# Kernel tuning notes

Hardware: AMD Instinct MI355X
Metric: run time of the kernel (lower is better)

## Reference

```python
import jax, jax.numpy as jnp
import numpy as np

E = 512
H = 8
SL = (16, 16, 16)
B = 4
LEN = np.array([768, 640, 704, 600], dtype=np.int32)


def _starts(lengths):
    cs = jnp.cumsum(lengths)
    starts = jnp.concatenate([jnp.zeros((1,), cs.dtype), cs[:-1]])
    return starts, cs


def _tile_within(data, lengths, buffer):
    # per-token causal window [cur, cur-1, ..., cur-L]; slots before sample start come from buffer
    L = buffer.shape[0]
    N = data.shape[0]
    starts, cs = _starts(lengths)
    g = jnp.arange(N)
    sid = jnp.searchsorted(cs, g, side='right')
    qpos = g - starts[sid]
    src = qpos[:, None] - jnp.arange(L + 1)[None, :]  # [N, L+1]
    from_data = src >= 0
    didx = jnp.clip(starts[sid][:, None] + src, 0, N - 1)
    bidx = jnp.clip(L + src, 0, L - 1)
    return jnp.where(from_data[:, :, None], data[didx], buffer[bidx])


def _mlp(h, w1, b1, w2, b2):
    return jax.nn.gelu(h @ w1 + b1, approximate=False) @ w2 + b2


def _selection(eu, lengths, win):
    # faithful port of the no_grad selection block (B > 1 branch)
    N = eu.shape[0]
    starts, _ = _starts(lengths)
    ends = starts + lengths - 1
    running = jnp.cumsum(eu)
    end_u = running[ends]
    sample_u = jnp.concatenate([end_u[:1], end_u[2:] - end_u[1:-1]])
    running = running - jnp.cumsum(jnp.zeros((N,), eu.dtype).at[starts[1:]].set(sample_u))
    offs = jnp.cumsum(jnp.zeros((N,), eu.dtype).at[starts[1:]].set(lengths[:-1].astype(eu.dtype)))
    idxs = jnp.arange(1, N + 1, dtype=eu.dtype) - offs
    selected = (eu > running / idxs) | (idxs <= win)
    csel = jnp.cumsum(selected.astype(jnp.int32))
    end_counts = csel[ends]
    next_lengths = jnp.concatenate([end_counts[:1], end_counts[1:] - end_counts[:-1]])
    take_map = csel - csel[0]  # unique_consecutive inverse of a 0/1-increment cumsum
    return jnp.nonzero(selected)[0], next_lengths, take_map


def _forward(args, lengths, sels):
    (x, kv_w, kv_b, q_w, q_b, proj_w, proj_b, buf0, buf1, buf2,
     d0_w1, d0_b1, d0_w2, d0_b2, d1_w1, d1_b1, d1_w2, d1_b2,
     u0_w1, u0_b1, u0_w2, u0_b2, u1_w1, u1_b1, u1_w2, u1_b2,
     wq, bq, wk, bk, wv, bv, out_w, out_b) = args
    Ls = [int(v) for v in np.asarray(lengths)]
    x_flat = jnp.concatenate([x[b, :Ls[b]] for b in range(len(Ls))])  # [N0, E]
    kv0 = x_flat @ kv_w + kv_b  # [N0, 2E]
    # scale 0
    tiled0 = _tile_within(kv0, lengths, buf0)  # [N0, SL0, 2E]
    eu0 = jax.nn.elu(_mlp(tiled0.reshape(tiled0.shape[0], -1), u0_w1, u0_b1, u0_w2, u0_b2))[:, 0] + 1.0
    s0 = _selection(jax.lax.stop_gradient(eu0), lengths, SL[0]) if sels is None else sels[0]
    sel0, len1, tm0 = s0
    selt0 = jnp.take(tiled0, sel0, 0)
    r0 = jax.nn.softmax(_mlp(selt0.reshape(selt0.shape[0], -1), d0_w1, d0_b1, d0_w2, d0_b2), -1)
    dat1 = jnp.sum(selt0 * r0[:, :, None], -2)  # [N1, 2E]
    util0 = _tile_within(jnp.take(eu0, sel0, 0)[:, None], len1, jnp.zeros((SL[1] - 1, 1), eu0.dtype))
    # scale 1
    tiled1 = _tile_within(dat1, len1, buf1)  # [N1, SL1, 2E]
    eu1 = jax.nn.elu(_mlp(tiled1.reshape(tiled1.shape[0], -1), u1_w1, u1_b1, u1_w2, u1_b2))[:, 0] + 1.0
    s1 = _selection(jax.lax.stop_gradient(eu1), len1, SL[1]) if sels is None else sels[1]
    sel1, len2, tm1 = s1
    selt1 = jnp.take(tiled1, sel1, 0)
    r1 = jax.nn.softmax(_mlp(selt1.reshape(selt1.shape[0], -1), d1_w1, d1_b1, d1_w2, d1_b2), -1)
    dat2 = jnp.sum(selt1 * r1[:, :, None], -2)  # [N2, 2E]
    util1 = _tile_within(jnp.take(eu1, sel1, 0)[:, None], len2, jnp.zeros((SL[2] - 1, 1), eu1.dtype))
    tiled2 = _tile_within(dat2, len2, buf2)  # [N2, SL2, 2E]
    # per-token multi-scale kv context (reconstructed tail of truncated forward)
    idx1 = tm0
    idx2 = jnp.take(tm1, idx1)
    win1 = jnp.take(tiled1, idx1, 0) * jnp.take(util0, idx1, 0)
    win2 = jnp.take(tiled2, idx2, 0) * jnp.take(util1, idx2, 0)
    kv = jnp.concatenate([tiled0, win1, win2], 1)  # [N0, sum(SL), 2E]
    k = kv[..., :E]
    v = kv[..., E:]
    q = x_flat @ q_w + q_b
    N0 = q.shape[0]
    Skv = kv.shape[1]
    hd = E // H
    qh = (q @ wq + bq).reshape(N0, H, hd)
    kh = (k @ wk + bk).reshape(N0, Skv, H, hd)
    vh = (v @ wv + bv).reshape(N0, Skv, H, hd)
    attn = jax.nn.softmax(jnp.einsum('nhd,nshd->nhs', qh, kh) / float(np.sqrt(hd)), -1)
    ctx = jnp.einsum('nhs,nshd->nhd', attn, vh).reshape(N0, E)
    y = (ctx @ out_w + out_b) @ proj_w + proj_b  # dropout in eval mode == identity
    out = jnp.zeros((len(Ls), max(Ls), E), y.dtype)
    off = 0
    for b, Lb in enumerate(Ls):
        out = out.at[b, :Lb].set(y[off:off + Lb])
        off += Lb
    return out, (s0, s1)


def setup_inputs():
    ks = list(jax.random.split(jax.random.key(0), 64))
    it = iter(ks)

    def nrm(shape, s=0.02):
        return jax.random.normal(next(it), shape, jnp.float32) * s

    def uni(shape):
        return jax.random.uniform(next(it), shape, dtype=jnp.float32)

    F = 2 * E
    inp = {
        'x': jax.random.normal(next(it), (B, int(LEN.max()), E), jnp.float32),
        'lengths': jnp.array(LEN),
        'kv_w': nrm((E, F)), 'kv_b': jnp.zeros((F,), jnp.float32),
        'q_w': nrm((E, E)), 'q_b': jnp.zeros((E,), jnp.float32),
        'proj_w': nrm((E, E)), 'proj_b': jnp.zeros((E,), jnp.float32),
        'buf0': uni((SL[0] - 1, F)), 'buf1': uni((SL[1] - 1, F)), 'buf2': uni((SL[2] - 1, F)),
    }
    for li in (0, 1):
        sl = SL[li]
        din, hid = sl * F, sl * 10
        inp['d%d_w1' % li] = nrm((din, hid)); inp['d%d_b1' % li] = jnp.zeros((hid,), jnp.float32)
        inp['d%d_w2' % li] = nrm((hid, sl)); inp['d%d_b2' % li] = jnp.zeros((sl,), jnp.float32)
        inp['u%d_w1' % li] = nrm((din, hid)); inp['u%d_b1' % li] = jnp.zeros((hid,), jnp.float32)
        inp['u%d_w2' % li] = nrm((hid, 1)); inp['u%d_b2' % li] = jnp.zeros((1,), jnp.float32)
    inp.update({'wq': nrm((E, E)), 'bq': jnp.zeros((E,), jnp.float32),
                'wk': nrm((E, E)), 'bk': jnp.zeros((E,), jnp.float32),
                'wv': nrm((E, E)), 'bv': jnp.zeros((E,), jnp.float32),
                'out_w': nrm((E, E)), 'out_b': jnp.zeros((E,), jnp.float32)})
    return inp


def reference(x, lengths, kv_w, kv_b, q_w, q_b, proj_w, proj_b, buf0, buf1, buf2,
              d0_w1, d0_b1, d0_w2, d0_b2, d1_w1, d1_b1, d1_w2, d1_b2,
              u0_w1, u0_b1, u0_w2, u0_b2, u1_w1, u1_b1, u1_w2, u1_b2,
              wq, bq, wk, bk, wv, bv, out_w, out_b):
    args = (x, kv_w, kv_b, q_w, q_b, proj_w, proj_b, buf0, buf1, buf2,
            d0_w1, d0_b1, d0_w2, d0_b2, d1_w1, d1_b1, d1_w2, d1_b2,
            u0_w1, u0_b1, u0_w2, u0_b2, u1_w1, u1_b1, u1_w2, u1_b2,
            wq, bq, wk, bk, wv, bv, out_w, out_b)
    out, _ = _forward(args, lengths, None)
    return out
```

## Files before the change

### kernel.cpp

```cpp
#include <hip/hip_runtime.h>
#include <cstddef>

#define DEVFN __device__ __forceinline__

constexpr int N0   = 2712;
constexpr int MAXL = 768;
constexpr int NBAT = 4;
constexpr int E    = 512;
constexpr int F    = 1024;
constexpr int HID  = 160;
constexpr int WSZ  = 16;
constexpr int NY   = 2 * WSZ * HID;
constexpr int XSTR = 2560;
constexpr size_t NOFF = (size_t)-1;

constexpr size_t oXF    = 0;
constexpr size_t oXO    = oXF    + (size_t)N0*E;
constexpr size_t oEU0   = oXO    + (size_t)N0*XSTR;
constexpr size_t oDAT1  = oEU0   + (size_t)N0;
constexpr size_t oEU1   = oDAT1  + (size_t)N0*F;
constexpr size_t oDAT2  = oEU1   + (size_t)N0;
constexpr size_t oBH0K  = oDAT2  + (size_t)N0*F;
constexpr size_t oBH0V  = oBH0K  + (size_t)15*E;
constexpr size_t oDH1K  = oBH0V  + (size_t)15*E;
constexpr size_t oDH1V  = oDH1K  + (size_t)N0*E;
constexpr size_t oDH2K  = oDH1V  + (size_t)N0*E;
constexpr size_t oDH2V  = oDH2K  + (size_t)N0*E;
constexpr size_t oCTX   = oDH2V  + (size_t)N0*E;
constexpr size_t oY2    = oCTX   + (size_t)N0*E;
constexpr size_t oEUS0  = oY2    + (size_t)N0*E;
constexpr size_t oEUS1  = oEUS0  + (size_t)N0;
constexpr size_t oSEL0  = oEUS1  + (size_t)N0;
constexpr size_t oTM0   = oSEL0  + (size_t)N0;
constexpr size_t oSEL1  = oTM0   + (size_t)N0;
constexpr size_t oTM1   = oSEL1  + (size_t)N0;
constexpr size_t oB0    = oTM1   + (size_t)N0;
constexpr size_t oB1    = oB0    + 8;
constexpr size_t oB2    = oB1    + 8;
constexpr size_t oWOP   = oB2    + 8;
constexpr size_t oBOP   = oWOP   + (size_t)E*E;
constexpr size_t oWX    = oBOP   + E;
constexpr size_t oXB    = oWX    + (size_t)E*XSTR;
constexpr size_t oBD0   = oXB    + XSTR;
constexpr size_t oBD1   = oBD0   + (size_t)F*NY;
constexpr size_t oBUFY0 = oBD1   + (size_t)F*NY;
constexpr size_t oBUFY1 = oBUFY0 + (size_t)15*NY;
constexpr size_t oYB    = oBUFY1 + (size_t)15*NY;
constexpr size_t oEND   = oYB    + (size_t)N0*NY;

__device__ float g_pool[oEND];

DEVFN float geluf(float x) {
    return 0.5f * x * (1.0f + erff(x / 1.41421356237309504880f));
}

__global__ void k_init() {
    if (threadIdx.x == 0) {
        int* b = (int*)(g_pool + oB0);
        b[0] = 0; b[1] = 768; b[2] = 1408; b[3] = 2112; b[4] = N0;
    }
}

__global__ __launch_bounds__(256) void k_xflat(const float* __restrict__ x) {
    int idx = blockIdx.x * 256 + threadIdx.x;
    if (idx >= N0 * E) return;
    int d = idx & (E - 1);
    int g = idx >> 9;
    int s = (g >= 768) + (g >= 1408) + (g >= 2112);
    const int st[4] = {0, 768, 1408, 2112};
    int qp = g - st[s];
    g_pool[oXF + idx] = x[((size_t)s * MAXL + qp) * E + d];
}

__global__ __launch_bounds__(256) void k_reshape(
    const float* __restrict__ uw, const float* __restrict__ dw, size_t bdOff)
{
    int idx = blockIdx.x * 256 + threadIdx.x;
    if (idx >= F * NY) return;
    int col = idx % NY;
    int f = idx / NY;
    const float* src = (col < NY / 2) ? uw : dw;
    int rem = (col < NY / 2) ? col : col - NY / 2;
    int j = rem / HID, n = rem % HID;
    g_pool[bdOff + idx] = src[((size_t)j * F + f) * HID + n];
}

__global__ __launch_bounds__(256) void k_copymat(
    const float* __restrict__ src, size_t dstOff, int rows, int cols, int lds, int ldd)
{
    int idx = blockIdx.x * 256 + threadIdx.x;
    if (idx >= rows * cols) return;
    int r = idx / cols, c = idx % cols;
    g_pool[dstOff + (size_t)r * ldd + c] = src[(size_t)r * lds + c];
}

__global__ __launch_bounds__(256) void k_prepvec(
    const float* __restrict__ kv_b, const float* __restrict__ q_b, const float* __restrict__ out_b,
    const float* __restrict__ wk, const float* __restrict__ bk,
    const float* __restrict__ wv, const float* __restrict__ bv,
    const float* __restrict__ wq, const float* __restrict__ bq,
    const float* __restrict__ proj_w, const float* __restrict__ proj_b)
{
    int idx = blockIdx.x * 256 + threadIdx.x;
    if (idx >= 3072) return;
    if (idx < 1024) { g_pool[oXB + idx] = kv_b[idx]; return; }
    const float* vec; const float* W; const float* add; int n; size_t dst;
    if (idx < 1536)      { n = idx - 1024; vec = kv_b;     W = wk;     add = bk;     dst = oXB + idx; }
    else if (idx < 2048) { n = idx - 1536; vec = kv_b + E; W = wv;     add = bv;     dst = oXB + idx; }
    else if (idx < 2560) { n = idx - 2048; vec = q_b;      W = wq;     add = bq;     dst = oXB + idx; }
    else                 { n = idx - 2560; vec = out_b;    W = proj_w; add = proj_b; dst = oBOP + n; }
    float s = add[n];
    for (int k = 0; k < E; ++k) s = fmaf(vec[k], W[(size_t)k * E + n], s);
    g_pool[dst] = s;
}

DEVFN void gemm64_body(
    const float* __restrict__ A, int lda,
    const float* __restrict__ B, int ldb,
    const float* __restrict__ bias,
    float* __restrict__ C, int ldc,
    int mval, int row0, int col0, int K, int N)
{
    __shared__ __align__(16) float As[32][68];
    __shared__ __align__(16) float Bs[32][64];

    int tid = threadIdx.x;
    float acc[4][4] = {};
    int tx = tid & 15, ty = tid >> 4;

    for (int k0 = 0; k0 < K; k0 += 32) {
        #pragma unroll
        for (int l = 0; l < 8; ++l) {
            int idx = tid + l * 256;
            int kk = idx & 31, m = idx >> 5;
            int r = row0 + m;
            float v = 0.0f;
            if (r < mval) v = A[(size_t)r * lda + k0 + kk];
            As[kk][m] = v;
        }
        #pragma unroll
        for (int l = 0; l < 8; ++l) {
            int idx = tid + l * 256;
            int n = idx & 63, kk = idx >> 6;
            int col = col0 + n;
            float v = 0.0f;
            if (col < N) v = B[(size_t)(k0 + kk) * ldb + col];
            Bs[kk][n] = v;
        }
        __syncthreads();
        #pragma unroll
        for (int kk = 0; kk < 32; ++kk) {
            float4 a4 = *(const float4*)&As[kk][ty * 4];
            float4 b4 = *(const float4*)&Bs[kk][tx * 4];
            float av[4] = {a4.x, a4.y, a4.z, a4.w};
            float bv[4] = {b4.x, b4.y, b4.z, b4.w};
            #pragma unroll
            for (int i = 0; i < 4; ++i)
                #pragma unroll
                for (int jn = 0; jn < 4; ++jn)
                    acc[i][jn] = fmaf(av[i], bv[jn], acc[i][jn]);
        }
        __syncthreads();
    }

    #pragma unroll
    for (int i = 0; i < 4; ++i) {
        int r = row0 + ty * 4 + i;
        if (r >= mval) continue;
        #pragma unroll
        for (int jn = 0; jn < 4; ++jn) {
            int col = col0 + tx * 4 + jn;
            if (col < N)
                C[(size_t)r * ldc + col] = acc[i][jn] + (bias ? bias[col] : 0.0f);
        }
    }
}

__global__ __launch_bounds__(256) void k_pgemm(
    size_t Aoff, int lda, size_t Boff, int ldb, size_t biasOff,
    size_t Coff, int ldc, int M, size_t mdevOff, int K, int N)
{
    int mval = (mdevOff == NOFF) ? M : *(const int*)(g_pool + mdevOff);
    int row0 = blockIdx.x * 64, col0 = blockIdx.y * 64;
    if (row0 >= mval) return;
    gemm64_body(g_pool + Aoff, lda, g_pool + Boff, ldb,
                (biasOff == NOFF) ? nullptr : g_pool + biasOff,
                g_pool + Coff, ldc, mval, row0, col0, K, N);
}

__global__ __launch_bounds__(256) void k_wprep(
    const float* __restrict__ kv_w, const float* __restrict__ q_w, const float* __restrict__ out_w,
    const float* __restrict__ wk, const float* __restrict__ wv,
    const float* __restrict__ wq, const float* __restrict__ proj_w)
{
    int z = blockIdx.z;
    const float* A; int lda; const float* B; float* C; int ldc;
    if (z == 0)      { A = kv_w;     lda = F; B = wk;     C = g_pool + oWX + 1024; ldc = XSTR; }
    else if (z == 1) { A = kv_w + E; lda = F; B = wv;     C = g_pool + oWX + 1536; ldc = XSTR; }
    else if (z == 2) { A = q_w;      lda = E; B = wq;     C = g_pool + oWX + 2048; ldc = XSTR; }
    else             { A = out_w;    lda = E; B = proj_w; C = g_pool + oWOP;       ldc = E;    }
    gemm64_body(A, lda, B, E, nullptr, C, ldc, E, blockIdx.x * 64, blockIdx.y * 64, E, E);
}

__global__ __launch_bounds__(256) void k_bufy(
    const float* __restrict__ buf0, const float* __restrict__ buf1)
{
    int z = blockIdx.z;
    const float* A = z ? buf1 : buf0;
    const float* B = g_pool + (z ? oBD1 : oBD0);
    float* C = g_pool + (z ? oBUFY1 : oBUFY0);
    gemm64_body(A, F, B, NY, nullptr, C, NY, 15, 0, blockIdx.y * 64, F, NY);
}

__global__ __launch_bounds__(256) void k_bh(
    const float* __restrict__ buf0,
    const float* __restrict__ wk, const float* __restrict__ bk,
    const float* __restrict__ wv, const float* __restrict__ bv)
{
    int z = blockIdx.z;
    const float* A = buf0 + (size_t)z * E;
    const float* B = z ? wv : wk;
    const float* bias = z ? bv : bk;
    float* C = g_pool + (z ? oBH0V : oBH0K);
    gemm64_body(A, F, B, E, bias, C, E, 15, 0, blockIdx.y * 64, E, E);
}

DEVFN void gemm128_body(
    const float* __restrict__ A, int lda,
    const float* __restrict__ B, int ldb,
    const float* __restrict__ bias,
    float* __restrict__ C, int ldc,
    int mval, int row0, int col0, int K)
{
    __shared__ __align__(16) float As[16][132];
    __shared__ __align__(16) float Bs[16][128];

    int tid = threadIdx.x;
    int tx = tid & 15, ty = tid >> 4;
    float acc[16][8] = {};

    for (int k0 = 0; k0 < K; k0 += 16) {
        #pragma unroll
        for (int l = 0; l < 4; ++l) {
            int idx = tid + l * 128;
            int r = idx >> 2, kq = (idx & 3) * 4;
            float4 v = make_float4(0.f, 0.f, 0.f, 0.f);
            int rr = row0 + r;
            if (rr < mval) v = *(const float4*)&A[(size_t)rr * lda + k0 + kq];
            As[kq][r] = v.x; As[kq + 1][r] = v.y; As[kq + 2][r] = v.z; As[kq + 3][r] = v.w;
        }
        #pragma unroll
        for (int l = 0; l < 4; ++l) {
            int idx = tid + l * 128;
            int k = idx >> 5, nq = (idx & 31) * 4;
            *(float4*)&Bs[k][nq] = *(const float4*)&B[(size_t)(k0 + k) * ldb + col0 + nq];
        }
        __syncthreads();
        #pragma unroll
        for (int kk = 0; kk < 16; ++kk) {
            float a0[16], b0[8];
            *(float4*)&a0[0]  = *(const float4*)&As[kk][ty * 16];
            *(float4*)&a0[4]  = *(const float4*)&As[kk][ty * 16 + 4];
            *(float4*)&a0[8]  = *(const float4*)&As[kk][ty * 16 + 8];
            *(float4*)&a0[12] = *(const float4*)&As[kk][ty * 16 + 12];
            *(float4*)&b0[0] = *(const float4*)&Bs[kk][tx * 4];
            *(float4*)&b0[4] = *(const float4*)&Bs[kk][64 + tx * 4];
            #pragma unroll
            for (int i = 0; i < 16; ++i)
                #pragma unroll
                for (int jn = 0; jn < 8; ++jn)
                    acc[i][jn] = fmaf(a0[i], b0[jn], acc[i][jn]);
        }
        __syncthreads();
    }

    #pragma unroll
    for (int i = 0; i < 16; ++i) {
        int r = row0 + ty * 16 + i;
        if (r >= mval) continue;
        float o0[4], o1[4];
        #pragma unroll
        for (int jn = 0; jn < 4; ++jn) {
            o0[jn] = acc[i][jn]     + (bias ? bias[col0 + tx * 4 + jn]      : 0.0f);
            o1[jn] = acc[i][jn + 4] + (bias ? bias[col0 + 64 + tx * 4 + jn] : 0.0f);
        }
        *(float4*)&C[(size_t)r * ldc + col0 + tx * 4]      = *(float4*)&o0[0];
        *(float4*)&C[(size_t)r * ldc + col0 + 64 + tx * 4] = *(float4*)&o1[0];
    }
}

__global__ __launch_bounds__(128, 2) void k_tgemm(
    size_t Aoff, int lda, size_t Boff, int ldb, size_t biasOff,
    size_t Coff, int ldc, int M, size_t mdevOff, int K)
{
    int mval = (mdevOff == NOFF) ? M : *(const int*)(g_pool + mdevOff);
    int row0 = blockIdx.x * 128, col0 = blockIdx.y * 128;
    if (row0 >= mval) return;
    gemm128_body(g_pool + Aoff, lda, g_pool + Boff, ldb,
                 (biasOff == NOFF) ? nullptr : g_pool + biasOff,
                 g_pool + Coff, ldc, mval, row0, col0, K);
}

__global__ __launch_bounds__(256) void k_zgemm(
    const float* __restrict__ wk, const float* __restrict__ wv)
{
    int z = blockIdx.z;
    int mval = *(const int*)(g_pool + ((z < 2) ? (oB1 + 4) : (oB2 + 4)));
    int row0 = blockIdx.x * 64, col0 = blockIdx.y * 64;
    if (row0 >= mval) return;
    const float* A = g_pool + ((z < 2) ? oDAT1 : oDAT2) + (size_t)(z & 1) * E;
    const float* B = (z & 1) ? wv : wk;
    float* C = g_pool + oDH1K + (size_t)z * N0 * E;
    gemm64_body(A, F, B, E, nullptr, C, E, mval, row0, col0, E, E);
}

__global__ void k_huev(
    size_t boundsOff, size_t bufYOff,
    const float* __restrict__ b1, const float* __restrict__ w2, const float* __restrict__ b2,
    size_t euOff, size_t mdevOff, int M)
{
    int i = blockIdx.x;
    int mval = (mdevOff == NOFF) ? M : *(const int*)(g_pool + mdevOff);
    if (i >= mval) return;
    int n = threadIdx.x;

    __shared__ float t[HID];
    const int* bounds = (const int*)(g_pool + boundsOff);
    int b1i = bounds[1], b2i = bounds[2], b3i = bounds[3];
    int s = (i >= b1i) + (i >= b2i) + (i >= b3i);
    int st = (s == 0) ? 0 : ((s == 1) ? b1i : ((s == 2) ? b2i : b3i));
    int qp = i - st;

    const float* Y = g_pool + oYB;
    const float* bufY = g_pool + bufYOff;

    if (n < HID) {
        float acc = b1[n];
        #pragma unroll
        for (int j = 0; j < WSZ; ++j) {
            int sp = qp - j;
            const float* row = (sp >= 0) ? &Y[(size_t)(i - j) * NY]
                                         : &bufY[(size_t)(15 + sp) * NY];
            acc += row[j * HID + n];
        }
        t[n] = geluf(acc) * w2[n];
    }
    __syncthreads();
    if (n == 0) {
        float v = b2[0];
        for (int k = 0; k < HID; ++k) v += t[k];
        v = (v > 0.0f) ? v : expm1f(v);
        g_pool[euOff + i] = v + 1.0f;
    }
}

__global__ __launch_bounds__(256) void k_select(
    size_t euOff, size_t boundsOff, int win,
    size_t selOff, size_t tmOff, size_t euSelOff, size_t boundsNextOff)
{
    __shared__ __align__(16) float se[N0];
    __shared__ __align__(16) float run[N0];
    __shared__ int sFlag[N0];
    __shared__ int sSum[256];
    __shared__ float sCz[NBAT];
    __shared__ int sEc[NBAT];
    __shared__ int sB[5];

    int tid = threadIdx.x;
    const int* bounds = (const int*)(g_pool + boundsOff);
    if (tid < 5) sB[tid] = bounds[tid];
    __syncthreads();
    int N = sB[4];
    for (int i = tid; i < N; i += 256) se[i] = g_pool[euOff + i];
    __syncthreads();

    if (tid == 0) {
        float r = 0.0f;
        int g = 0;
        for (; g + 8 <= N; g += 8) {
            float4 a = *(const float4*)&se[g];
            float4 b4 = *(const float4*)&se[g + 4];
            r += a.x;  run[g]     = r;
            r += a.y;  run[g + 1] = r;
            r += a.z;  run[g + 2] = r;
            r += a.w;  run[g + 3] = r;
            r += b4.x; run[g + 4] = r;
            r += b4.y; run[g + 5] = r;
            r += b4.z; run[g + 6] = r;
            r += b4.w; run[g + 7] = r;
        }
        for (; g < N; ++g) { r += se[g]; run[g] = r; }
        float e0 = run[sB[1] - 1], e1 = run[sB[2] - 1], e2 = run[sB[3] - 1];
        float su0 = e0;
        float su1 = e2 - e1;
        float su2 = run[sB[4] - 1] - e2;
        sCz[0] = 0.0f;
        sCz[1] = su0;
        sCz[2] = su0 + su1;
        sCz[3] = (su0 + su1) + su2;
    }
    __syncthreads();

    for (int g = tid; g < N; g += 256) {
        int seg = (g >= sB[1]) + (g >= sB[2]) + (g >= sB[3]);
        int st = (seg == 0) ? 0 : sB[seg];
        int qp1 = g - st + 1;
        float r2 = run[g] - sCz[seg];
        bool seld = (se[g] > r2 / (float)qp1) || (qp1 <= win);
        sFlag[g] = seld ? 1 : 0;
    }
    __syncthreads();

    int CH = (N + 255) >> 8;
    int lo = tid * CH, hi = min(lo + CH, N);
    {
        int s = 0;
        for (int g = lo; g < hi; ++g) s += sFlag[g];
        sSum[tid] = s;
    }
    __syncthreads();
    if (tid == 0) {
        int acc = 0;
        for (int t = 0; t < 256; ++t) { int v = sSum[t]; sSum[t] = acc; acc += v; }
    }
    __syncthreads();

    int* sel = (int*)(g_pool + selOff);
    int* tm  = (int*)(g_pool + tmOff);
    float* eus = g_pool + euSelOff;
    int* bn  = (int*)(g_pool + boundsNextOff);

    int csel0 = sFlag[0];
    {
        int csel = sSum[tid];
        for (int g = lo; g < hi; ++g) {
            csel += sFlag[g];
            tm[g] = csel - csel0;
            if (sFlag[g]) { sel[csel - 1] = g; eus[csel - 1] = se[g]; }
            #pragma unroll
            for (int s = 0; s < NBAT; ++s)
                if (g == sB[s + 1] - 1) sEc[s] = csel;
        }
    }
    __syncthreads();
    if (tid == 0) {
        bn[0] = 0; bn[1] = sEc[0]; bn[2] = sEc[1]; bn[3] = sEc[2]; bn[4] = sEc[3];
    }
}

__global__ __launch_bounds__(256) void k_rdat(
    size_t boundsOff, size_t bufYOff,
    const float* __restrict__ b1, const float* __restrict__ w2, const float* __restrict__ b2,
    size_t selOff, size_t mdevOff,
    size_t srcOff, int srcStr, const float* __restrict__ buf,
    size_t datOff)
{
    int i = blockIdx.x;
    if (i >= *(const int*)(g_pool + mdevOff)) return;
    const float* src = g_pool + srcOff;
    const int* bounds = (const int*)(g_pool + boundsOff);
    const int* sel = (const int*)(g_pool + selOff);
    float* dat = g_pool + datOff;

    __shared__ float gh[HID];
    __shared__ float sv[WSZ];
    __shared__ float r[WSZ];
    __shared__ int sG, sQp;

    int tid = threadIdx.x;
    if (tid == 0) {
        int g = sel[i];
        int b1i = bounds[1], b2i = bounds[2], b3i = bounds[3];
        int s = (g >= b1i) + (g >= b2i) + (g >= b3i);
        int st = (s == 0) ? 0 : ((s == 1) ? b1i : ((s == 2) ? b2i : b3i));
        sG = g; sQp = g - st;
    }
    __syncthreads();
    int g = sG, qp = sQp;

    if (tid < HID) {
        const float* Y = g_pool + oYB;
        const float* bufY = g_pool + bufYOff;
        float acc = b1[tid];
        #pragma unroll
        for (int j = 0; j < WSZ; ++j) {
            int sp = qp - j;
            const float* row = (sp >= 0) ? &Y[(size_t)(g - j) * NY]
                                         : &bufY[(size_t)(15 + sp) * NY];
            acc += row[NY / 2 + j * HID + tid];
        }
        gh[tid] = geluf(acc);
    }
    __syncthreads();
    if (tid < WSZ) {
        float acc = 0.0f;
        for (int k = 0; k < HID; ++k) acc += gh[k] * w2[k * WSZ + tid];
        sv[tid] = acc + b2[tid];
    }
    __syncthreads();
    if (tid == 0) {
        float m = sv[0];
        for (int t = 1; t < WSZ; ++t) m = fmaxf(m, sv[t]);
        float sum = 0.0f;
        for (int t = 0; t < WSZ; ++t) { float e = expf(sv[t] - m); r[t] = e; sum += e; }
        for (int t = 0; t < WSZ; ++t) r[t] = r[t] / sum;
    }
    __syncthreads();
    for (int f = tid; f < F; f += 256) {
        float acc = 0.0f;
        for (int j = 0; j < WSZ; ++j) {
            int sp = qp - j;
            float v = (sp >= 0) ? src[(size_t)(g - j) * srcStr + f]
                                : buf[(size_t)(15 + sp) * F + f];
            acc = fmaf(r[j], v, acc);
        }
        dat[(size_t)i * F + f] = acc;
    }
}

__global__ __launch_bounds__(512) void k_attn(
    const float* __restrict__ bk, const float* __restrict__ bv)
{
    int g = blockIdx.x;
    const float* XO   = g_pool + oXO;
    const float* BH0k = g_pool + oBH0K;
    const float* BH0v = g_pool + oBH0V;
    const float* DH1k = g_pool + oDH1K;
    const float* DH1v = g_pool + oDH1V;
    const float* DH2k = g_pool + oDH2K;
    const float* DH2v = g_pool + oDH2V;
    const float* eus0 = g_pool + oEUS0;
    const float* eus1 = g_pool + oEUS1;
    const int* tm0 = (const int*)(g_pool + oTM0);
    const int* tm1 = (const int*)(g_pool + oTM1);
    const int* bounds1 = (const int*)(g_pool + oB1);
    const int* bounds2 = (const int*)(g_pool + oB2);

    __shared__ const float* sK[48];
    __shared__ const float* sV[48];
    __shared__ float sScale[48];
    __shared__ __align__(16) float sQ[E], sBk[E], sBv[E];
    __shared__ float sc[48][8];

    int tid = threadIdx.x;
    sQ[tid]  = XO[(size_t)g * XSTR + 2048 + tid];
    sBk[tid] = bk[tid];
    sBv[tid] = bv[tid];

    if (tid < 48) {
        int s = tid;
        const float *pK = nullptr, *pV = nullptr;
        float scl = 0.0f;
        if (s < 16) {
            int s0 = (g >= 768) + (g >= 1408) + (g >= 2112);
            const int st0[4] = {0, 768, 1408, 2112};
            int sp = (g - st0[s0]) - s;
            if (sp >= 0) { pK = XO + (size_t)(g - s) * XSTR + 1024; pV = XO + (size_t)(g - s) * XSTR + 1536; }
            else         { pK = BH0k + (size_t)(15 + sp) * E; pV = BH0v + (size_t)(15 + sp) * E; }
            scl = 1.0f;
        } else if (s < 32) {
            int j = s - 16;
            int i1 = tm0[g];
            int b1 = bounds1[1], b2 = bounds1[2], b3 = bounds1[3];
            int sg = (i1 >= b1) + (i1 >= b2) + (i1 >= b3);
            int st = (sg == 0) ? 0 : ((sg == 1) ? b1 : ((sg == 2) ? b2 : b3));
            int sp = (i1 - st) - j;
            if (sp >= 0) { pK = DH1k + (size_t)(i1 - j) * E; pV = DH1v + (size_t)(i1 - j) * E; scl = eus0[i1 - j]; }
        } else {
            int j = s - 32;
            int i1 = tm0[g];
            int i2 = tm1[i1];
            int b1 = bounds2[1], b2 = bounds2[2], b3 = bounds2[3];
            int sg = (i2 >= b1) + (i2 >= b2) + (i2 >= b3);
            int st = (sg == 0) ? 0 : ((sg == 1) ? b1 : ((sg == 2) ? b2 : b3));
            int sp = (i2 - st) - j;
            if (sp >= 0) { pK = DH2k + (size_t)(i2 - j) * E; pV = DH2v + (size_t)(i2 - j) * E; scl = eus1[i2 - j]; }
        }
        sK[s] = pK; sV[s] = pV; sScale[s] = scl;
    }
    __syncthreads();

    if (tid < 384) {
        int s = tid >> 3, h = tid & 7;
        const float* bp = sK[s];
        float scl = sScale[s];
        float acc = 0.0f;
        int d0 = h * 64;
        if (s < 16) {
            for (int d = 0; d < 64; d += 4) {
                float4 qv = *(const float4*)&sQ[d0 + d];
                float4 kv4 = *(const float4*)&bp[d0 + d];
                acc += qv.x * kv4.x; acc += qv.y * kv4.y;
                acc += qv.z * kv4.z; acc += qv.w * kv4.w;
            }
        } else if (bp) {
            for (int d = 0; d < 64; d += 4) {
                float4 qv = *(const float4*)&sQ[d0 + d];
                float4 kv4 = *(const float4*)&bp[d0 + d];
                float4 bb = *(const float4*)&sBk[d0 + d];
                acc += qv.x * (bb.x + scl * kv4.x); acc += qv.y * (bb.y + scl * kv4.y);
                acc += qv.z * (bb.z + scl * kv4.z); acc += qv.w * (bb.w + scl * kv4.w);
            }
        } else {
            for (int d = 0; d < 64; d += 4) {
                float4 qv = *(const float4*)&sQ[d0 + d];
                float4 bb = *(const float4*)&sBk[d0 + d];
                acc += qv.x * bb.x; acc += qv.y * bb.y;
                acc += qv.z * bb.z; acc += qv.w * bb.w;
            }
        }
        sc[s][h] = acc * 0.125f;
    }
    __syncthreads();

    if (tid < 8) {
        int h = tid;
        float m = sc[0][h];
        for (int s = 1; s < 48; ++s) m = fmaxf(m, sc[s][h]);
        float sum = 0.0f;
        for (int s = 0; s < 48; ++s) { float e = expf(sc[s][h] - m); sc[s][h] = e; sum += e; }
        for (int s = 0; s < 48; ++s) sc[s][h] = sc[s][h] / sum;
    }
    __syncthreads();

    {
        int d = tid, h = d >> 6;
        float acc = 0.0f;
        for (int s = 0; s < 48; ++s) {
            const float* bp = sV[s];
            float vv;
            if (s < 16) vv = bp[d];
            else        vv = sBv[d] + (bp ? sScale[s] * bp[d] : 0.0f);
            acc = fmaf(sc[s][h], vv, acc);
        }
        g_pool[oCTX + (size_t)g * E + d] = acc;
    }
}

__global__ __launch_bounds__(256) void k_scatter(float* __restrict__ out) {
    int idx = blockIdx.x * 256 + threadIdx.x;
    if (idx >= NBAT * MAXL * E) return;
    int d = idx & (E - 1);
    int rest = idx >> 9;
    int p = rest % MAXL, bb = rest / MAXL;
    const int st[4] = {0, 768, 1408, 2112};
    const int ln[4] = {768, 640, 704, 600};
    out[idx] = (p < ln[bb]) ? g_pool[oY2 + (size_t)(st[bb] + p) * E + d] : 0.0f;
}

extern "C" void kernel_launch(void* const* d_in, const int* in_sizes, int n_in,
                              void* d_out, int out_size, void* d_ws, size_t ws_size,
                              hipStream_t stream)
{
    (void)in_sizes; (void)n_in; (void)d_ws; (void)ws_size; (void)out_size;

    const float* x      = (const float*)d_in[0];
    const float* kv_w   = (const float*)d_in[2];
    const float* kv_b   = (const float*)d_in[3];
    const float* q_w    = (const float*)d_in[4];
    const float* q_b    = (const float*)d_in[5];
    const float* proj_w = (const float*)d_in[6];
    const float* proj_b = (const float*)d_in[7];
    const float* buf0   = (const float*)d_in[8];
    const float* buf1   = (const float*)d_in[9];
    const float* d0_w1  = (const float*)d_in[11];
    const float* d0_b1  = (const float*)d_in[12];
    const float* d0_w2  = (const float*)d_in[13];
    const float* d0_b2  = (const float*)d_in[14];
    const float* u0_w1  = (const float*)d_in[15];
    const float* u0_b1  = (const float*)d_in[16];
    const float* u0_w2  = (const float*)d_in[17];
    const float* u0_b2  = (const float*)d_in[18];
    const float* d1_w1  = (const float*)d_in[19];
    const float* d1_b1  = (const float*)d_in[20];
    const float* d1_w2  = (const float*)d_in[21];
    const float* d1_b2  = (const float*)d_in[22];
    const float* u1_w1  = (const float*)d_in[23];
    const float* u1_b1  = (const float*)d_in[24];
    const float* u1_w2  = (const float*)d_in[25];
    const float* u1_b2  = (const float*)d_in[26];
    const float* wq     = (const float*)d_in[27];
    const float* bq     = (const float*)d_in[28];
    const float* wk     = (const float*)d_in[29];
    const float* bk     = (const float*)d_in[30];
    const float* wv     = (const float*)d_in[31];
    const float* bv     = (const float*)d_in[32];
    const float* out_w  = (const float*)d_in[33];
    const float* out_b  = (const float*)d_in[34];

    auto cdiv = [](int a, int b) { return (a + b - 1) / b; };
    auto GT = [&](int M, int N) { return dim3(cdiv(M, 128), cdiv(N, 128)); };

    k_init<<<1, 64, 0, stream>>>();
    k_xflat<<<cdiv(N0 * E, 256), 256, 0, stream>>>(x);

    k_reshape<<<cdiv(F * NY, 256), 256, 0, stream>>>(u0_w1, d0_w1, oBD0);
    k_reshape<<<cdiv(F * NY, 256), 256, 0, stream>>>(u1_w1, d1_w1, oBD1);
    k_copymat<<<cdiv(E * F, 256), 256, 0, stream>>>(kv_w, oWX, E, F, F, XSTR);
    k_wprep<<<dim3(8, 8, 4), 256, 0, stream>>>(kv_w, q_w, out_w, wk, wv, wq, proj_w);
    k_prepvec<<<cdiv(3072, 256), 256, 0, stream>>>(kv_b, q_b, out_b, wk, bk, wv, bv, wq, bq, proj_w, proj_b);
    k_bufy<<<dim3(1, NY / 64, 2), 256, 0, stream>>>(buf0, buf1);
    k_bh<<<dim3(1, E / 64, 2), 256, 0, stream>>>(buf0, wk, bk, wv, bv);

    k_tgemm<<<GT(N0, XSTR), 128, 0, stream>>>(oXF, E, oWX, XSTR, oXB, oXO, XSTR, N0, NOFF, E);

    k_tgemm<<<GT(N0, NY), 128, 0, stream>>>(oXO, XSTR, oBD0, NY, NOFF, oYB, NY, N0, NOFF, F);
    k_huev<<<N0, 160, 0, stream>>>(oB0, oBUFY0, u0_b1, u0_w2, u0_b2, oEU0, NOFF, N0);
    k_select<<<1, 256, 0, stream>>>(oEU0, oB0, WSZ, oSEL0, oTM0, oEUS0, oB1);
    k_rdat<<<N0, 256, 0, stream>>>(oB0, oBUFY0, d0_b1, d0_w2, d0_b2, oSEL0, oB1 + 4, oXO, XSTR, buf0, oDAT1);

    k_tgemm<<<GT(N0, NY), 128, 0, stream>>>(oDAT1, F, oBD1, NY, NOFF, oYB, NY, N0, oB1 + 4, F);
    k_huev<<<N0, 160, 0, stream>>>(oB1, oBUFY1, u1_b1, u1_w2, u1_b2, oEU1, oB1 + 4, N0);
    k_select<<<1, 256, 0, stream>>>(oEU1, oB1, WSZ, oSEL1, oTM1, oEUS1, oB2);
    k_rdat<<<N0, 256, 0, stream>>>(oB1, oBUFY1, d1_b1, d1_w2, d1_b2, oSEL1, oB2 + 4, oDAT1, F, buf1, oDAT2);

    k_zgemm<<<dim3(cdiv(N0, 64), E / 64, 4), 256, 0, stream>>>(wk, wv);

    k_attn<<<N0, 512, 0, stream>>>(bk, bv);
    k_pgemm<<<dim3(cdiv(N0, 64), E / 64), 256, 0, stream>>>(oCTX, E, oWOP, E, oBOP, oY2, E, N0, NOFF, E, E);
    k_scatter<<<cdiv(NBAT * MAXL * E, 256), 256, 0, stream>>>((float*)d_out);
}
```

Before: 1.562 ms.

## Retile 128x128 GEMM to 256 threads with 8x8 per-thread tiles and register prefetch

```diff
diff --git a/kernel.cpp b/kernel.cpp
--- a/kernel.cpp
+++ b/kernel.cpp
@@ -225,6 +225,22 @@
     gemm64_body(A, F, B, E, bias, C, E, 15, 0, blockIdx.y * 64, E, E);
 }
 
+DEVFN void fma_8x8(const float4& a0, const float4& a1, const float4& b0, const float4& b1,
+                   float2 (&acc)[8][4])
+{
+    float av[8] = {a0.x, a0.y, a0.z, a0.w, a1.x, a1.y, a1.z, a1.w};
+    float2 bv[4] = {make_float2(b0.x, b0.y), make_float2(b0.z, b0.w),
+                    make_float2(b1.x, b1.y), make_float2(b1.z, b1.w)};
+    #pragma unroll
+    for (int i = 0; i < 8; ++i) {
+        #pragma unroll
+        for (int q = 0; q < 4; ++q) {
+            acc[i][q].x = fmaf(av[i], bv[q].x, acc[i][q].x);
+            acc[i][q].y = fmaf(av[i], bv[q].y, acc[i][q].y);
+        }
+    }
+}
+
 DEVFN void gemm128_body(
     const float* __restrict__ A, int lda,
     const float* __restrict__ B, int ldb,
@@ -233,63 +249,77 @@
     int mval, int row0, int col0, int K)
 {
     __shared__ __align__(16) float As[16][132];
-    __shared__ __align__(16) float Bs[16][128];
+    __shared__ __align__(16) float Bs[16][132];
 
     int tid = threadIdx.x;
     int tx = tid & 15, ty = tid >> 4;
-    float acc[16][8] = {};
+    float2 acc[8][4] = {};
+
+    int ar = tid >> 1, akq = (tid & 1) * 8;
+    int bk = tid >> 4, bnq = (tid & 15) * 8;
 
     for (int k0 = 0; k0 < K; k0 += 16) {
+        {
+            float4 v0 = make_float4(0.f, 0.f, 0.f, 0.f), v1 = v0;
+            int rr = row0 + ar;
+            if (rr < mval) {
+                v0 = *(const float4*)&A[(size_t)rr * lda + k0 + akq];
+                v1 = *(const float4*)&A[(size_t)rr * lda + k0 + akq + 4];
+            }
+            As[akq + 0][ar] = v0.x; As[akq + 1][ar] = v0.y;
+            As[akq + 2][ar] = v0.z; As[akq + 3][ar] = v0.w;
+            As[akq + 4][ar] = v1.x; As[akq + 5][ar] = v1.y;
+            As[akq + 6][ar] = v1.z; As[akq + 7][ar] = v1.w;
+        }
+        {
+            const float* bp = &B[(size_t)(k0 + bk) * ldb + col0 + bnq];
+            *(float4*)&Bs[bk][bnq]     = *(const float4*)&bp[0];
+            *(float4*)&Bs[bk][bnq + 4] = *(const float4*)&bp[4];
+        }
+        __syncthreads();
+
+        float4 a0A = *(const float4*)&As[0][ty * 8];
+        float4 a1A = *(const float4*)&As[0][ty * 8 + 4];
+        float4 b0A = *(const float4*)&Bs[0][tx * 4];
+        float4 b1A = *(const float4*)&Bs[0][64 + tx * 4];
         #pragma unroll
-        for (int l = 0; l < 4; ++l) {
-            int idx = tid + l * 128;
-            int r = idx >> 2, kq = (idx & 3) * 4;
-            float4 v = make_float4(0.f, 0.f, 0.f, 0.f);
-            int rr = row0 + r;
-            if (rr < mval) v = *(const float4*)&A[(size_t)rr * lda + k0 + kq];
-            As[kq][r] = v.x; As[kq + 1][r] = v.y; As[kq + 2][r] = v.z; As[kq + 3][r] = v.w;
-        }
-        #pragma unroll
-        for (int l = 0; l < 4; ++l) {
-            int idx = tid + l * 128;
-            int k = idx >> 5, nq = (idx & 31) * 4;
-            *(float4*)&Bs[k][nq] = *(const float4*)&B[(size_t)(k0 + k) * ldb + col0 + nq];
+        for (int kk = 0; kk < 16; kk += 2) {
+            float4 a0B = *(const float4*)&As[kk + 1][ty * 8];
+            float4 a1B = *(const float4*)&As[kk + 1][ty * 8 + 4];
+            float4 b0B = *(const float4*)&Bs[kk + 1][tx * 4];
+            float4 b1B = *(const float4*)&Bs[kk + 1][64 + tx * 4];
+            fma_8x8(a0A, a1A, b0A, b1A, acc);
+            if (kk + 2 < 16) {
+                a0A = *(const float4*)&As[kk + 2][ty * 8];
+                a1A = *(const float4*)&As[kk + 2][ty * 8 + 4];
+                b0A = *(const float4*)&Bs[kk + 2][tx * 4];
+                b1A = *(const float4*)&Bs[kk + 2][64 + tx * 4];
+            }
+            fma_8x8(a0B, a1B, b0B, b1B, acc);
         }
         __syncthreads();
-        #pragma unroll
-        for (int kk = 0; kk < 16; ++kk) {
-            float a0[16], b0[8];
-            *(float4*)&a0[0]  = *(const float4*)&As[kk][ty * 16];
-            *(float4*)&a0[4]  = *(const float4*)&As[kk][ty * 16 + 4];
-            *(float4*)&a0[8]  = *(const float4*)&As[kk][ty * 16 + 8];
-            *(float4*)&a0[12] = *(const float4*)&As[kk][ty * 16 + 12];
-            *(float4*)&b0[0] = *(const float4*)&Bs[kk][tx * 4];
-            *(float4*)&b0[4] = *(const float4*)&Bs[kk][64 + tx * 4];
-            #pragma unroll
-            for (int i = 0; i < 16; ++i)
-                #pragma unroll
-                for (int jn = 0; jn < 8; ++jn)
-                    acc[i][jn] = fmaf(a0[i], b0[jn], acc[i][jn]);
-        }
-        __syncthreads();
     }
 
     #pragma unroll
-    for (int i = 0; i < 16; ++i) {
-        int r = row0 + ty * 16 + i;
+    for (int i = 0; i < 8; ++i) {
+        int r = row0 + ty * 8 + i;
         if (r >= mval) continue;
         float o0[4], o1[4];
-        #pragma unroll
-        for (int jn = 0; jn < 4; ++jn) {
-            o0[jn] = acc[i][jn]     + (bias ? bias[col0 + tx * 4 + jn]      : 0.0f);
-            o1[jn] = acc[i][jn + 4] + (bias ? bias[col0 + 64 + tx * 4 + jn] : 0.0f);
+        o0[0] = acc[i][0].x; o0[1] = acc[i][0].y; o0[2] = acc[i][1].x; o0[3] = acc[i][1].y;
+        o1[0] = acc[i][2].x; o1[1] = acc[i][2].y; o1[2] = acc[i][3].x; o1[3] = acc[i][3].y;
+        if (bias) {
+            #pragma unroll
+            for (int jn = 0; jn < 4; ++jn) {
+                o0[jn] += bias[col0 + tx * 4 + jn];
+                o1[jn] += bias[col0 + 64 + tx * 4 + jn];
+            }
         }
         *(float4*)&C[(size_t)r * ldc + col0 + tx * 4]      = *(float4*)&o0[0];
         *(float4*)&C[(size_t)r * ldc + col0 + 64 + tx * 4] = *(float4*)&o1[0];
     }
 }
 
-__global__ __launch_bounds__(128, 2) void k_tgemm(
+__global__ __launch_bounds__(256) void k_tgemm(
     size_t Aoff, int lda, size_t Boff, int ldb, size_t biasOff,
     size_t Coff, int ldc, int M, size_t mdevOff, int K)
 {
@@ -702,14 +732,14 @@
     k_bufy<<<dim3(1, NY / 64, 2), 256, 0, stream>>>(buf0, buf1);
     k_bh<<<dim3(1, E / 64, 2), 256, 0, stream>>>(buf0, wk, bk, wv, bv);
 
-    k_tgemm<<<GT(N0, XSTR), 128, 0, stream>>>(oXF, E, oWX, XSTR, oXB, oXO, XSTR, N0, NOFF, E);
-
-    k_tgemm<<<GT(N0, NY), 128, 0, stream>>>(oXO, XSTR, oBD0, NY, NOFF, oYB, NY, N0, NOFF, F);
+    k_tgemm<<<GT(N0, XSTR), 256, 0, stream>>>(oXF, E, oWX, XSTR, oXB, oXO, XSTR, N0, NOFF, E);
+
+    k_tgemm<<<GT(N0, NY), 256, 0, stream>>>(oXO, XSTR, oBD0, NY, NOFF, oYB, NY, N0, NOFF, F);
     k_huev<<<N0, 160, 0, stream>>>(oB0, oBUFY0, u0_b1, u0_w2, u0_b2, oEU0, NOFF, N0);
     k_select<<<1, 256, 0, stream>>>(oEU0, oB0, WSZ, oSEL0, oTM0, oEUS0, oB1);
     k_rdat<<<N0, 256, 0, stream>>>(oB0, oBUFY0, d0_b1, d0_w2, d0_b2, oSEL0, oB1 + 4, oXO, XSTR, buf0, oDAT1);
 
-    k_tgemm<<<GT(N0, NY), 128, 0, stream>>>(oDAT1, F, oBD1, NY, NOFF, oYB, NY, N0, oB1 + 4, F);
+    k_tgemm<<<GT(N0, NY), 256, 0, stream>>>(oDAT1, F, oBD1, NY, NOFF, oYB, NY, N0, oB1 + 4, F);
     k_huev<<<N0, 160, 0, stream>>>(oB1, oBUFY1, u1_b1, u1_w2, u1_b2, oEU1, oB1 + 4, N0);
     k_select<<<1, 256, 0, stream>>>(oEU1, oB1, WSZ, oSEL1, oTM1, oEUS1, oB2);
     k_rdat<<<N0, 256, 0, stream>>>(oB1, oBUFY1, d1_b1, d1_w2, d1_b2, oSEL1, oB2 + 4, oDAT1, F, buf1, oDAT2);
```

After: 1.380 ms. 11.7% less time.
